# Kernel optimization log

Measured on AMD Instinct MI355X. Metric: run time of the kernel, lower is better.

## Reference

```python
import jax, jax.numpy as jnp
import numpy as np

DIM = 512
NUM_HEAD = 8
HEAD_DIM = DIM // NUM_HEAD
FFN = 4 * DIM


def setup_inputs() -> dict:
    key = jax.random.key(0)
    ks = jax.random.split(key, 16)
    s = DIM ** -0.5
    inp = {
        "x": jax.random.normal(ks[0], (4, 2048, DIM), jnp.float32),
        "wq": jax.random.normal(ks[1], (DIM, DIM), jnp.float32) * s,
        "bq": jnp.zeros((DIM,), jnp.float32),
        "wk": jax.random.normal(ks[2], (DIM, DIM), jnp.float32) * s,
        "bk": jnp.zeros((DIM,), jnp.float32),
        "wv": jax.random.normal(ks[3], (DIM, DIM), jnp.float32) * s,
        "bv": jnp.zeros((DIM,), jnp.float32),
        "wo": jax.random.normal(ks[4], (DIM, DIM), jnp.float32) * s,
        "bo": jnp.zeros((DIM,), jnp.float32),
        "w1": jax.random.normal(ks[5], (DIM, FFN), jnp.float32) * s,
        "b1": jnp.zeros((FFN,), jnp.float32),
        "w2": jax.random.normal(ks[6], (FFN, DIM), jnp.float32) * (FFN ** -0.5),
        "b2": jnp.zeros((DIM,), jnp.float32),
        "g1": jnp.ones((DIM,), jnp.float32),
        "be1": jnp.zeros((DIM,), jnp.float32),
        "g2": jnp.ones((DIM,), jnp.float32),
        "be2": jnp.zeros((DIM,), jnp.float32),
    }
    return inp


def layer_norm(x, g, b, eps=1e-5):
    mu = jnp.mean(x, axis=-1, keepdims=True)
    var = jnp.var(x, axis=-1, keepdims=True)
    return (x - mu) * jax.lax.rsqrt(var + eps) * g + b


def _forward(x, wq, bq, wk, bk, wv, bv, wo, bo, w1, b1, w2, b2, g1, be1, g2, be2):
    b, n, _ = x.shape
    scale = HEAD_DIM ** -0.5
    q = (x @ wq + bq).reshape(b, n, NUM_HEAD, HEAD_DIM).transpose(0, 2, 1, 3)
    k = (x @ wk + bk).reshape(b, n, NUM_HEAD, HEAD_DIM).transpose(0, 2, 1, 3)
    v = (x @ wv + bv).reshape(b, n, NUM_HEAD, HEAD_DIM).transpose(0, 2, 1, 3)
    scores = jnp.einsum('bhqd,bhkd->bhqk', q, k) * scale
    attn = jax.nn.softmax(scores, axis=-1)
    out = jnp.einsum('bhqk,bhkd->bhqd', attn, v)
    out = out.transpose(0, 2, 1, 3).reshape(b, n, DIM)
    out = out @ wo + bo
    x = layer_norm(out + x, g1, be1)
    h = jax.nn.gelu(x @ w1 + b1, approximate=False)
    ff = h @ w2 + b2
    x = layer_norm(ff + x, g2, be2)
    return x


def reference(x, wq, bq, wk, bk, wv, bv, wo, bo, w1, b1, w2, b2, g1, be1, g2, be2):
    return _forward(x, wq, bq, wk, bk, wv, bv, wo, bo, w1, b1, w2, b2, g1, be1, g2, be2)
```

## Files before the change

### kernel.cpp

```cpp
#include <hip/hip_runtime.h>
#include <math.h>

#define DIM 512
#define NHEAD 8
#define HD 64
#define FFN_DIM 2048
#define BATCH 4
#define SEQ 2048
#define MTOK (BATCH*SEQ)

typedef __attribute__((ext_vector_type(8))) short bf16x8;
typedef __attribute__((ext_vector_type(4))) float f32x4;

__device__ __forceinline__ unsigned short f2b(float f){
    unsigned int u = __float_as_uint(f);
    u += 0x7fffu + ((u >> 16) & 1u);
    return (unsigned short)(u >> 16);
}
__device__ __forceinline__ float b2f(unsigned short u){
    return __uint_as_float(((unsigned int)u) << 16);
}
__device__ __forceinline__ unsigned int pack_trunc(float f0, float f1){
    return __builtin_amdgcn_perm(__float_as_uint(f1), __float_as_uint(f0), 0x07060302u);
}
__device__ __forceinline__ void async_cp16(const unsigned short* g, unsigned short* l){
    __builtin_amdgcn_global_load_lds((const __attribute__((address_space(1))) unsigned int*)g,
                                     (__attribute__((address_space(3))) unsigned int*)l, 16, 0, 0);
}

__device__ __forceinline__ void transp32(const float* __restrict__ in, unsigned short* __restrict__ out,
                                         int N, int K, int n0_rd, int n0_wr, int k0,
                                         unsigned short (&t)[32][33], int tid){
    int tx = tid & 31, ty = tid >> 5;
    #pragma unroll
    for (int u = 0; u < 4; u++)
        t[tx][ty + 8*u] = f2b(in[(size_t)(k0 + ty + 8*u)*N + n0_rd + tx]);
    __syncthreads();
    #pragma unroll
    for (int u = 0; u < 4; u++)
        out[(size_t)(n0_wr + ty + 8*u)*K + k0 + tx] = t[ty + 8*u][tx];
}

__global__ void prep_kernel(const float* __restrict__ x,
                            const float* __restrict__ wq, const float* __restrict__ wk,
                            const float* __restrict__ wv, const float* __restrict__ wo,
                            const float* __restrict__ w1, const float* __restrict__ w2,
                            const float* __restrict__ bq, const float* __restrict__ bk,
                            const float* __restrict__ bv,
                            unsigned short* __restrict__ xb, unsigned short* __restrict__ wqkvT,
                            unsigned short* __restrict__ woT, unsigned short* __restrict__ w1T,
                            unsigned short* __restrict__ w2T, float* __restrict__ bqkv)
{
    __shared__ unsigned short t[32][33];
    int bid = blockIdx.x, tid = threadIdx.x;
    if (bid < 4096) {
        int i = (bid*256 + tid)*4;
        float4 v = *(const float4*)(x + i);
        ushort4 o; o.x=f2b(v.x); o.y=f2b(v.y); o.z=f2b(v.z); o.w=f2b(v.w);
        *(ushort4*)(xb + i) = o;
    } else if (bid < 4864) {
        int r = bid - 4096;
        int n0 = (r % 48)*32, k0 = (r / 48)*32;
        const float* w = (n0 < 512) ? wq : (n0 < 1024) ? wk : wv;
        transp32(w, wqkvT, 512, 512, n0 & 511, n0, k0, t, tid);
    } else if (bid < 5120) {
        int r = bid - 4864;
        int n0 = (r % 16)*32, k0 = (r / 16)*32;
        transp32(wo, woT, 512, 512, n0, n0, k0, t, tid);
    } else if (bid < 6144) {
        int r = bid - 5120;
        int n0 = (r % 64)*32, k0 = (r / 64)*32;
        transp32(w1, w1T, 2048, 512, n0, n0, k0, t, tid);
    } else if (bid < 7168) {
        int r = bid - 6144;
        int n0 = (r % 16)*32, k0 = (r / 16)*32;
        transp32(w2, w2T, 512, 2048, n0, n0, k0, t, tid);
    } else {
        int i = (bid - 7168)*256 + tid;
        if (i < 1536)
            bqkv[i] = (i < 512) ? bq[i] : (i < 1024) ? bk[i-512] : bv[i-1024];
    }
}

template<int MODE, int TN, int SK>
__global__ __launch_bounds__(256)
void gemm_bf16(const unsigned short* __restrict__ A, const unsigned short* __restrict__ Bt,
               const float* __restrict__ bias,
               float* __restrict__ Cf, unsigned short* __restrict__ Cb,
               unsigned short* __restrict__ qo, unsigned short* __restrict__ ko,
               unsigned short* __restrict__ vTo,
               int M, int N, int K)
{
    constexpr int JN = (TN == 128) ? 4 : 2;
    __shared__ unsigned short As[128*64];
    __shared__ unsigned short Bs[TN*64];
    int tid  = threadIdx.x;
    int lane = tid & 63;
    int ln = lane & 15, qd = lane >> 4;
    int m0 = blockIdx.x * 128, n0 = blockIdx.y * TN;
    int wid = tid >> 6;
    int wm = (wid >> 1) * 64;
    int wn = (wid & 1) * (16*JN);
    int kbeg = (SK > 1) ? (int)blockIdx.z * (K/SK) : 0;
    int kend = kbeg + K/SK;
    if (SK > 1) Cf += (size_t)blockIdx.z * M * N;

    f32x4 acc[4][JN];
    #pragma unroll
    for (int i = 0; i < 4; i++)
        #pragma unroll
        for (int j = 0; j < JN; j++) acc[i][j] = (f32x4){0.f,0.f,0.f,0.f};

    for (int k0 = kbeg; k0 < kend; k0 += 64) {
        #pragma unroll
        for (int i = 0; i < 4; i++) {
            int cid = i*256 + tid;
            int row = cid >> 3, cs = cid & 7;
            int cg = cs ^ (row & 7);
            async_cp16(&A[(size_t)(m0+row)*K + k0 + cg*8], &As[(cid & ~63) * 8]);
        }
        #pragma unroll
        for (int i = 0; i < TN/32; i++) {
            int cid = i*256 + tid;
            int row = cid >> 3, cs = cid & 7;
            int cg = cs ^ (row & 7);
            async_cp16(&Bt[(size_t)(n0+row)*K + k0 + cg*8], &Bs[(cid & ~63) * 8]);
        }
        __syncthreads();
        #pragma unroll
        for (int kk = 0; kk < 64; kk += 32) {
            int c0 = kk >> 3;
            bf16x8 af[4], bf[JN];
            #pragma unroll
            for (int t = 0; t < 4; t++)
                af[t] = *(bf16x8*)&As[(wm + t*16 + ln)*64 + ((c0 + qd) ^ (ln & 7))*8];
            #pragma unroll
            for (int t = 0; t < JN; t++)
                bf[t] = *(bf16x8*)&Bs[(wn + t*16 + ln)*64 + ((c0 + qd) ^ (ln & 7))*8];
            #pragma unroll
            for (int i = 0; i < 4; i++)
                #pragma unroll
                for (int j = 0; j < JN; j++)
                    acc[i][j] = __builtin_amdgcn_mfma_f32_16x16x32_bf16(af[i], bf[j], acc[i][j], 0,0,0);
        }
        __syncthreads();
    }

    const float QSCALE = 0.18033688011112042f;
    #pragma unroll
    for (int i = 0; i < 4; i++) {
        int mb = m0 + wm + i*16 + qd*4;
        #pragma unroll
        for (int j = 0; j < JN; j++) {
            int c = n0 + wn + j*16 + ln;
            float bv_ = (SK > 1 && blockIdx.z) ? 0.f : bias[c];
            float v[4];
            #pragma unroll
            for (int r = 0; r < 4; r++) v[r] = acc[i][j][r] + bv_;
            if (MODE == 0) {
                #pragma unroll
                for (int r = 0; r < 4; r++) Cf[(size_t)(mb+r)*N + c] = v[r];
            } else if (MODE == 2) {
                #pragma unroll
                for (int r = 0; r < 4; r++) {
                    float g = 0.5f * v[r] * (1.0f + erff(v[r] * 0.70710678118654752f));
                    Cb[(size_t)(mb+r)*N + c] = f2b(g);
                }
            } else {
                int b = mb >> 11, t0 = mb & 2047;
                if (c < 512) {
                    int h = c >> 6, hd = c & 63;
                    #pragma unroll
                    for (int r = 0; r < 4; r++)
                        qo[(((size_t)(b*8 + h))*SEQ + t0 + r)*64 + hd] = f2b(v[r] * QSCALE);
                } else if (c < 1024) {
                    int cc = c - 512, h = cc >> 6, hd = cc & 63;
                    #pragma unroll
                    for (int r = 0; r < 4; r++)
                        ko[(((size_t)(b*8 + h))*SEQ + t0 + r)*64 + hd] = f2b(v[r]);
                } else {
                    int cc = c - 1024, h = cc >> 6, hd = cc & 63;
                    ushort4 pk;
                    pk.x = f2b(v[0]); pk.y = f2b(v[1]); pk.z = f2b(v[2]); pk.w = f2b(v[3]);
                    *(ushort4*)&vTo[(((size_t)(b*8 + h))*64 + hd)*SEQ + t0] = pk;
                }
            }
        }
    }
}

__global__ __launch_bounds__(256)
void attn_mfma(const unsigned short* __restrict__ Q, const unsigned short* __restrict__ K,
               const unsigned short* __restrict__ VT, unsigned short* __restrict__ O)
{
    __shared__ unsigned short lds[20480];
    unsigned short* Qs = lds + 8192;
    unsigned short* Ps = lds + 16384;
    int tid  = threadIdx.x;
    int wid  = tid >> 6, lane = tid & 63;
    int ln = lane & 15, qd = lane >> 4;
    int qb = blockIdx.x, bh = blockIdx.y;

    #pragma unroll
    for (int i = 0; i < 2; i++) {
        int cid = i*256 + tid;
        int row = cid >> 3, cs = cid & 7;
        int cg = cs ^ (row & 7);
        async_cp16(&Q [((size_t)bh*SEQ + qb*64 + row)*64 + cg*8], &Qs[(cid & ~63)*8]);
        async_cp16(&K [((size_t)bh*SEQ + row)*64 + cg*8],         &lds[(cid & ~63)*8]);
        async_cp16(&VT[((size_t)bh*64 + row)*SEQ + cg*8],         &lds[4096 + (cid & ~63)*8]);
    }
    __syncthreads();

    bf16x8 qf[2];
    #pragma unroll
    for (int kk = 0; kk < 2; kk++)
        qf[kk] = *(bf16x8*)&Qs[(wid*16 + ln)*64 + (((kk*4) + qd) ^ (ln & 7))*8];
    __syncthreads();

    f32x4 o[4];
    #pragma unroll
    for (int dt = 0; dt < 4; dt++) o[dt] = (f32x4){0.f,0.f,0.f,0.f};
    float l_i = 0.f;

    for (int kt = 0; kt < 32; kt++) {
        int kof = (kt & 1) * 8192;
        int vof = 4096 + kof;
        if (kt < 31) {
            int nkof = 8192 - kof;
            #pragma unroll
            for (int i = 0; i < 2; i++) {
                int cid = i*256 + tid;
                int row = cid >> 3, cs = cid & 7;
                int cg = cs ^ (row & 7);
                async_cp16(&K [((size_t)bh*SEQ + (kt+1)*64 + row)*64 + cg*8], &lds[nkof + (cid & ~63)*8]);
                async_cp16(&VT[((size_t)bh*64 + row)*SEQ + (kt+1)*64 + cg*8], &lds[nkof + 4096 + (cid & ~63)*8]);
            }
        }

        f32x4 s[4];
        #pragma unroll
        for (int nt = 0; nt < 4; nt++) s[nt] = (f32x4){0.f,0.f,0.f,0.f};
        #pragma unroll
        for (int kk = 0; kk < 64; kk += 32) {
            int c0 = kk >> 3;
            #pragma unroll
            for (int nt = 0; nt < 4; nt++) {
                bf16x8 kf = *(bf16x8*)&lds[kof + (nt*16 + ln)*64 + ((c0 + qd) ^ (ln & 7))*8];
                s[nt] = __builtin_amdgcn_mfma_f32_16x16x32_bf16(kf, qf[kk>>5], s[nt], 0,0,0);
            }
        }

        #pragma unroll
        for (int nt = 0; nt < 4; nt++) {
            #pragma unroll
            for (int r = 0; r < 4; r++) {
                float p = __builtin_amdgcn_exp2f(s[nt][r]);
                s[nt][r] = p;
                l_i += p;
            }
        }

        #pragma unroll
        for (int nt = 0; nt < 4; nt++) {
            uint2 pk;
            pk.x = pack_trunc(s[nt][0], s[nt][1]);
            pk.y = pack_trunc(s[nt][2], s[nt][3]);
            *(uint2*)&Ps[(wid*16 + ln)*64 + ((nt*2 + (qd>>1)) ^ (ln & 7))*8 + (qd&1)*4] = pk;
        }

        #pragma unroll
        for (int kk = 0; kk < 64; kk += 32) {
            int c0 = kk >> 3;
            bf16x8 pf = *(bf16x8*)&Ps[(wid*16 + ln)*64 + ((c0 + qd) ^ (ln & 7))*8];
            #pragma unroll
            for (int dt = 0; dt < 4; dt++) {
                bf16x8 vf = *(bf16x8*)&lds[vof + (dt*16 + ln)*64 + ((c0 + qd) ^ (ln & 7))*8];
                o[dt] = __builtin_amdgcn_mfma_f32_16x16x32_bf16(vf, pf, o[dt], 0,0,0);
            }
        }
        __syncthreads();
    }

    l_i += __shfl_xor(l_i, 16);
    l_i += __shfl_xor(l_i, 32);
    float linv = 1.0f / l_i;

    int b = bh >> 3, h = bh & 7;
    int t = qb*64 + wid*16 + ln;
    #pragma unroll
    for (int dt = 0; dt < 4; dt++) {
        ushort4 pk;
        pk.x = f2b(o[dt][0]*linv); pk.y = f2b(o[dt][1]*linv);
        pk.z = f2b(o[dt][2]*linv); pk.w = f2b(o[dt][3]*linv);
        *(ushort4*)&O[((size_t)b*SEQ + t)*DIM + h*64 + dt*16 + qd*4] = pk;
    }
}

__global__ void ln1_kernel(const float* __restrict__ mainp, const float* __restrict__ resp,
                           const float* __restrict__ g, const float* __restrict__ be,
                           unsigned short* __restrict__ outb)
{
    int row  = blockIdx.x*4 + (threadIdx.x >> 6);
    int lane = threadIdx.x & 63;
    size_t base = (size_t)row * DIM + lane*8;

    float4 m0 = *(const float4*)(mainp + base);
    float4 m1 = *(const float4*)(mainp + base + 4);
    float4 r0 = *(const float4*)(resp + base);
    float4 r1 = *(const float4*)(resp + base + 4);
    float v[8] = { m0.x+r0.x, m0.y+r0.y, m0.z+r0.z, m0.w+r0.w,
                   m1.x+r1.x, m1.y+r1.y, m1.z+r1.z, m1.w+r1.w };
    float s = 0.f, s2 = 0.f;
    #pragma unroll
    for (int i = 0; i < 8; i++) { s += v[i]; s2 += v[i]*v[i]; }
    #pragma unroll
    for (int d = 32; d >= 1; d >>= 1) { s += __shfl_xor(s, d); s2 += __shfl_xor(s2, d); }
    float mean = s * (1.0f / DIM);
    float rstd = rsqrtf(s2 * (1.0f / DIM) - mean*mean + 1e-5f);

    float4 g0 = *(const float4*)(g + lane*8);
    float4 g1 = *(const float4*)(g + lane*8 + 4);
    float4 b0 = *(const float4*)(be + lane*8);
    float4 b1 = *(const float4*)(be + lane*8 + 4);
    float gg[8] = {g0.x,g0.y,g0.z,g0.w,g1.x,g1.y,g1.z,g1.w};
    float bb[8] = {b0.x,b0.y,b0.z,b0.w,b1.x,b1.y,b1.z,b1.w};
    ushort4 p0, p1;
    float o0 = (v[0]-mean)*rstd*gg[0]+bb[0], o1 = (v[1]-mean)*rstd*gg[1]+bb[1];
    float o2 = (v[2]-mean)*rstd*gg[2]+bb[2], o3 = (v[3]-mean)*rstd*gg[3]+bb[3];
    float o4 = (v[4]-mean)*rstd*gg[4]+bb[4], o5 = (v[5]-mean)*rstd*gg[5]+bb[5];
    float o6 = (v[6]-mean)*rstd*gg[6]+bb[6], o7 = (v[7]-mean)*rstd*gg[7]+bb[7];
    p0.x=f2b(o0); p0.y=f2b(o1); p0.z=f2b(o2); p0.w=f2b(o3);
    p1.x=f2b(o4); p1.y=f2b(o5); p1.z=f2b(o6); p1.w=f2b(o7);
    *(ushort4*)(outb + base)     = p0;
    *(ushort4*)(outb + base + 4) = p1;
}

__global__ void ln2_kernel(const float* __restrict__ m0p, const float* __restrict__ m1p,
                           const unsigned short* __restrict__ resb,
                           const float* __restrict__ g, const float* __restrict__ be,
                           float* __restrict__ outf)
{
    int row  = blockIdx.x*4 + (threadIdx.x >> 6);
    int lane = threadIdx.x & 63;
    size_t base = (size_t)row * DIM + lane*8;

    float4 a0 = *(const float4*)(m0p + base);
    float4 a1 = *(const float4*)(m0p + base + 4);
    float4 c0 = *(const float4*)(m1p + base);
    float4 c1 = *(const float4*)(m1p + base + 4);
    ushort4 rb0 = *(const ushort4*)(resb + base);
    ushort4 rb1 = *(const ushort4*)(resb + base + 4);
    float v[8] = { a0.x+c0.x+b2f(rb0.x), a0.y+c0.y+b2f(rb0.y),
                   a0.z+c0.z+b2f(rb0.z), a0.w+c0.w+b2f(rb0.w),
                   a1.x+c1.x+b2f(rb1.x), a1.y+c1.y+b2f(rb1.y),
                   a1.z+c1.z+b2f(rb1.z), a1.w+c1.w+b2f(rb1.w) };
    float s = 0.f, s2 = 0.f;
    #pragma unroll
    for (int i = 0; i < 8; i++) { s += v[i]; s2 += v[i]*v[i]; }
    #pragma unroll
    for (int d = 32; d >= 1; d >>= 1) { s += __shfl_xor(s, d); s2 += __shfl_xor(s2, d); }
    float mean = s * (1.0f / DIM);
    float rstd = rsqrtf(s2 * (1.0f / DIM) - mean*mean + 1e-5f);

    float4 g0 = *(const float4*)(g + lane*8);
    float4 g1 = *(const float4*)(g + lane*8 + 4);
    float4 b0 = *(const float4*)(be + lane*8);
    float4 b1 = *(const float4*)(be + lane*8 + 4);
    float gg[8] = {g0.x,g0.y,g0.z,g0.w,g1.x,g1.y,g1.z,g1.w};
    float bb[8] = {b0.x,b0.y,b0.z,b0.w,b1.x,b1.y,b1.z,b1.w};
    float o[8];
    #pragma unroll
    for (int i = 0; i < 8; i++) o[i] = (v[i] - mean)*rstd*gg[i] + bb[i];
    *(float4*)(outf + base)     = (float4){o[0],o[1],o[2],o[3]};
    *(float4*)(outf + base + 4) = (float4){o[4],o[5],o[6],o[7]};
}

extern "C" void kernel_launch(void* const* d_in, const int* in_sizes, int n_in,
                              void* d_out, int out_size, void* d_ws, size_t ws_size,
                              hipStream_t stream) {
    const float* x   = (const float*)d_in[0];
    const float* wq  = (const float*)d_in[1];
    const float* bq  = (const float*)d_in[2];
    const float* wk  = (const float*)d_in[3];
    const float* bk  = (const float*)d_in[4];
    const float* wv  = (const float*)d_in[5];
    const float* bv  = (const float*)d_in[6];
    const float* wo  = (const float*)d_in[7];
    const float* bo  = (const float*)d_in[8];
    const float* w1  = (const float*)d_in[9];
    const float* b1  = (const float*)d_in[10];
    const float* w2  = (const float*)d_in[11];
    const float* b2  = (const float*)d_in[12];
    const float* g1  = (const float*)d_in[13];
    const float* be1 = (const float*)d_in[14];
    const float* g2  = (const float*)d_in[15];
    const float* be2 = (const float*)d_in[16];
    float* out = (float*)d_out;

    char* w = (char*)d_ws;
    size_t off = 0;
    auto alloc = [&](size_t bytes){ void* p = w + off; off += (bytes + 255) & ~(size_t)255; return p; };
    unsigned short* xb     = (unsigned short*)alloc((size_t)MTOK*DIM*2);
    unsigned short* wqkvT  = (unsigned short*)alloc((size_t)1536*512*2);
    unsigned short* woT    = (unsigned short*)alloc((size_t)512*512*2);
    unsigned short* w1T    = (unsigned short*)alloc((size_t)2048*512*2);
    unsigned short* w2T    = (unsigned short*)alloc((size_t)512*2048*2);
    float*          bqkv   = (float*)alloc(1536*4);
    unsigned short* qb_    = (unsigned short*)alloc((size_t)32*SEQ*64*2);
    unsigned short* kb_    = (unsigned short*)alloc((size_t)32*SEQ*64*2);
    unsigned short* vT_    = (unsigned short*)alloc((size_t)32*64*SEQ*2);
    unsigned short* attno  = (unsigned short*)alloc((size_t)MTOK*DIM*2);
    float*          aproj  = (float*)alloc((size_t)MTOK*DIM*4);
    unsigned short* x1b    = (unsigned short*)alloc((size_t)MTOK*DIM*2);
    unsigned short* h_     = (unsigned short*)alloc((size_t)MTOK*FFN_DIM*2);
    float*          ff     = (float*)alloc((size_t)2*MTOK*DIM*4);

    prep_kernel<<<7174, 256, 0, stream>>>(x, wq, wk, wv, wo, w1, w2, bq, bk, bv,
                                          xb, wqkvT, woT, w1T, w2T, bqkv);

    gemm_bf16<1,128,1><<<dim3(64,12), 256, 0, stream>>>(xb, wqkvT, bqkv, nullptr, nullptr,
                                                        qb_, kb_, vT_, MTOK, 1536, DIM);
    attn_mfma<<<dim3(32,32), 256, 0, stream>>>(qb_, kb_, vT_, attno);
    gemm_bf16<0,64,1><<<dim3(64,8), 256, 0, stream>>>(attno, woT, bo, aproj, nullptr,
                                                      nullptr, nullptr, nullptr, MTOK, DIM, DIM);
    ln1_kernel<<<MTOK/4, 256, 0, stream>>>(aproj, x, g1, be1, x1b);
    gemm_bf16<2,128,1><<<dim3(64,16), 256, 0, stream>>>(x1b, w1T, b1, nullptr, h_,
                                                        nullptr, nullptr, nullptr, MTOK, FFN_DIM, DIM);
    gemm_bf16<0,128,2><<<dim3(64,4,2), 256, 0, stream>>>(h_, w2T, b2, ff, nullptr,
                                                         nullptr, nullptr, nullptr, MTOK, DIM, FFN_DIM);
    ln2_kernel<<<MTOK/4, 256, 0, stream>>>(ff, ff + (size_t)MTOK*DIM, x1b, g2, be2, out);
}
```

Baseline: 278.5 us.

## Process 128 queries per attention block and split-K the output projection

The attention kernel now gives each wave two 16-row query sub-tiles, so every K and V fragment loaded from LDS feeds two MFMAs. This halves the grid and the K/V traffic per query. The output projection GEMM switches to the 128-tile split-K-by-2 variant that writes two partial buffers, and LN1 now sums both partials plus the residual. The cost is more registers per wave and fewer blocks in flight for attention, plus an extra fp32 partial read in LN1.

```diff
diff --git a/kernel.cpp b/kernel.cpp
--- a/kernel.cpp
+++ b/kernel.cpp
@@ -193,7 +193,7 @@
 void attn_mfma(const unsigned short* __restrict__ Q, const unsigned short* __restrict__ K,
                const unsigned short* __restrict__ VT, unsigned short* __restrict__ O)
 {
-    __shared__ unsigned short lds[20480];
+    __shared__ unsigned short lds[24576];
     unsigned short* Qs = lds + 8192;
     unsigned short* Ps = lds + 16384;
     int tid  = threadIdx.x;
@@ -202,26 +202,36 @@
     int qb = blockIdx.x, bh = blockIdx.y;
 
     #pragma unroll
+    for (int i = 0; i < 4; i++) {
+        int cid = i*256 + tid;
+        int row = cid >> 3, cs = cid & 7;
+        int cg = cs ^ (row & 7);
+        async_cp16(&Q[((size_t)bh*SEQ + qb*128 + row)*64 + cg*8], &Qs[(cid & ~63)*8]);
+    }
+    #pragma unroll
     for (int i = 0; i < 2; i++) {
         int cid = i*256 + tid;
         int row = cid >> 3, cs = cid & 7;
         int cg = cs ^ (row & 7);
-        async_cp16(&Q [((size_t)bh*SEQ + qb*64 + row)*64 + cg*8], &Qs[(cid & ~63)*8]);
-        async_cp16(&K [((size_t)bh*SEQ + row)*64 + cg*8],         &lds[(cid & ~63)*8]);
-        async_cp16(&VT[((size_t)bh*64 + row)*SEQ + cg*8],         &lds[4096 + (cid & ~63)*8]);
+        async_cp16(&K [((size_t)bh*SEQ + row)*64 + cg*8], &lds[(cid & ~63)*8]);
+        async_cp16(&VT[((size_t)bh*64 + row)*SEQ + cg*8], &lds[4096 + (cid & ~63)*8]);
     }
     __syncthreads();
 
-    bf16x8 qf[2];
-    #pragma unroll
-    for (int kk = 0; kk < 2; kk++)
-        qf[kk] = *(bf16x8*)&Qs[(wid*16 + ln)*64 + (((kk*4) + qd) ^ (ln & 7))*8];
+    bf16x8 qf[2][2];
+    #pragma unroll
+    for (int qs = 0; qs < 2; qs++)
+        #pragma unroll
+        for (int kk = 0; kk < 2; kk++)
+            qf[qs][kk] = *(bf16x8*)&Qs[(wid*32 + qs*16 + ln)*64 + ((kk*4 + qd) ^ (ln & 7))*8];
     __syncthreads();
 
-    f32x4 o[4];
-    #pragma unroll
-    for (int dt = 0; dt < 4; dt++) o[dt] = (f32x4){0.f,0.f,0.f,0.f};
-    float l_i = 0.f;
+    f32x4 o[2][4];
+    #pragma unroll
+    for (int qs = 0; qs < 2; qs++)
+        #pragma unroll
+        for (int dt = 0; dt < 4; dt++) o[qs][dt] = (f32x4){0.f,0.f,0.f,0.f};
+    float l_i[2] = {0.f, 0.f};
 
     for (int kt = 0; kt < 32; kt++) {
         int kof = (kt & 1) * 8192;
@@ -238,66 +248,72 @@
             }
         }
 
-        f32x4 s[4];
-        #pragma unroll
-        for (int nt = 0; nt < 4; nt++) s[nt] = (f32x4){0.f,0.f,0.f,0.f};
-        #pragma unroll
-        for (int kk = 0; kk < 64; kk += 32) {
-            int c0 = kk >> 3;
+        f32x4 s[2][4];
+        #pragma unroll
+        for (int qs = 0; qs < 2; qs++)
+            #pragma unroll
+            for (int nt = 0; nt < 4; nt++) s[qs][nt] = (f32x4){0.f,0.f,0.f,0.f};
+        #pragma unroll
+        for (int kk = 0; kk < 2; kk++) {
             #pragma unroll
             for (int nt = 0; nt < 4; nt++) {
-                bf16x8 kf = *(bf16x8*)&lds[kof + (nt*16 + ln)*64 + ((c0 + qd) ^ (ln & 7))*8];
-                s[nt] = __builtin_amdgcn_mfma_f32_16x16x32_bf16(kf, qf[kk>>5], s[nt], 0,0,0);
+                bf16x8 kf = *(bf16x8*)&lds[kof + (nt*16 + ln)*64 + ((kk*4 + qd) ^ (ln & 7))*8];
+                s[0][nt] = __builtin_amdgcn_mfma_f32_16x16x32_bf16(kf, qf[0][kk], s[0][nt], 0,0,0);
+                s[1][nt] = __builtin_amdgcn_mfma_f32_16x16x32_bf16(kf, qf[1][kk], s[1][nt], 0,0,0);
             }
         }
 
         #pragma unroll
-        for (int nt = 0; nt < 4; nt++) {
-            #pragma unroll
-            for (int r = 0; r < 4; r++) {
-                float p = __builtin_amdgcn_exp2f(s[nt][r]);
-                s[nt][r] = p;
-                l_i += p;
+        for (int qs = 0; qs < 2; qs++) {
+            #pragma unroll
+            for (int nt = 0; nt < 4; nt++) {
+                #pragma unroll
+                for (int r = 0; r < 4; r++) {
+                    float p = __builtin_amdgcn_exp2f(s[qs][nt][r]);
+                    s[qs][nt][r] = p;
+                    l_i[qs] += p;
+                }
+                uint2 pk;
+                pk.x = pack_trunc(s[qs][nt][0], s[qs][nt][1]);
+                pk.y = pack_trunc(s[qs][nt][2], s[qs][nt][3]);
+                *(uint2*)&Ps[(wid*32 + qs*16 + ln)*64 + ((nt*2 + (qd>>1)) ^ (ln & 7))*8 + (qd&1)*4] = pk;
             }
         }
 
         #pragma unroll
-        for (int nt = 0; nt < 4; nt++) {
-            uint2 pk;
-            pk.x = pack_trunc(s[nt][0], s[nt][1]);
-            pk.y = pack_trunc(s[nt][2], s[nt][3]);
-            *(uint2*)&Ps[(wid*16 + ln)*64 + ((nt*2 + (qd>>1)) ^ (ln & 7))*8 + (qd&1)*4] = pk;
-        }
-
-        #pragma unroll
-        for (int kk = 0; kk < 64; kk += 32) {
-            int c0 = kk >> 3;
-            bf16x8 pf = *(bf16x8*)&Ps[(wid*16 + ln)*64 + ((c0 + qd) ^ (ln & 7))*8];
+        for (int kk = 0; kk < 2; kk++) {
+            bf16x8 pf0 = *(bf16x8*)&Ps[(wid*32 + ln)*64      + ((kk*4 + qd) ^ (ln & 7))*8];
+            bf16x8 pf1 = *(bf16x8*)&Ps[(wid*32 + 16 + ln)*64 + ((kk*4 + qd) ^ (ln & 7))*8];
             #pragma unroll
             for (int dt = 0; dt < 4; dt++) {
-                bf16x8 vf = *(bf16x8*)&lds[vof + (dt*16 + ln)*64 + ((c0 + qd) ^ (ln & 7))*8];
-                o[dt] = __builtin_amdgcn_mfma_f32_16x16x32_bf16(vf, pf, o[dt], 0,0,0);
+                bf16x8 vf = *(bf16x8*)&lds[vof + (dt*16 + ln)*64 + ((kk*4 + qd) ^ (ln & 7))*8];
+                o[0][dt] = __builtin_amdgcn_mfma_f32_16x16x32_bf16(vf, pf0, o[0][dt], 0,0,0);
+                o[1][dt] = __builtin_amdgcn_mfma_f32_16x16x32_bf16(vf, pf1, o[1][dt], 0,0,0);
             }
         }
         __syncthreads();
     }
 
-    l_i += __shfl_xor(l_i, 16);
-    l_i += __shfl_xor(l_i, 32);
-    float linv = 1.0f / l_i;
-
     int b = bh >> 3, h = bh & 7;
-    int t = qb*64 + wid*16 + ln;
-    #pragma unroll
-    for (int dt = 0; dt < 4; dt++) {
-        ushort4 pk;
-        pk.x = f2b(o[dt][0]*linv); pk.y = f2b(o[dt][1]*linv);
-        pk.z = f2b(o[dt][2]*linv); pk.w = f2b(o[dt][3]*linv);
-        *(ushort4*)&O[((size_t)b*SEQ + t)*DIM + h*64 + dt*16 + qd*4] = pk;
-    }
-}
-
-__global__ void ln1_kernel(const float* __restrict__ mainp, const float* __restrict__ resp,
+    #pragma unroll
+    for (int qs = 0; qs < 2; qs++) {
+        float l = l_i[qs];
+        l += __shfl_xor(l, 16);
+        l += __shfl_xor(l, 32);
+        float linv = 1.0f / l;
+        int t = qb*128 + wid*32 + qs*16 + ln;
+        #pragma unroll
+        for (int dt = 0; dt < 4; dt++) {
+            ushort4 pk;
+            pk.x = f2b(o[qs][dt][0]*linv); pk.y = f2b(o[qs][dt][1]*linv);
+            pk.z = f2b(o[qs][dt][2]*linv); pk.w = f2b(o[qs][dt][3]*linv);
+            *(ushort4*)&O[((size_t)b*SEQ + t)*DIM + h*64 + dt*16 + qd*4] = pk;
+        }
+    }
+}
+
+__global__ void ln1_kernel(const float* __restrict__ m0p, const float* __restrict__ m1p,
+                           const float* __restrict__ resp,
                            const float* __restrict__ g, const float* __restrict__ be,
                            unsigned short* __restrict__ outb)
 {
@@ -305,12 +321,14 @@
     int lane = threadIdx.x & 63;
     size_t base = (size_t)row * DIM + lane*8;
 
-    float4 m0 = *(const float4*)(mainp + base);
-    float4 m1 = *(const float4*)(mainp + base + 4);
+    float4 a0 = *(const float4*)(m0p + base);
+    float4 a1 = *(const float4*)(m0p + base + 4);
+    float4 c0 = *(const float4*)(m1p + base);
+    float4 c1 = *(const float4*)(m1p + base + 4);
     float4 r0 = *(const float4*)(resp + base);
     float4 r1 = *(const float4*)(resp + base + 4);
-    float v[8] = { m0.x+r0.x, m0.y+r0.y, m0.z+r0.z, m0.w+r0.w,
-                   m1.x+r1.x, m1.y+r1.y, m1.z+r1.z, m1.w+r1.w };
+    float v[8] = { a0.x+c0.x+r0.x, a0.y+c0.y+r0.y, a0.z+c0.z+r0.z, a0.w+c0.w+r0.w,
+                   a1.x+c1.x+r1.x, a1.y+c1.y+r1.y, a1.z+c1.z+r1.z, a1.w+c1.w+r1.w };
     float s = 0.f, s2 = 0.f;
     #pragma unroll
     for (int i = 0; i < 8; i++) { s += v[i]; s2 += v[i]*v[i]; }
@@ -326,12 +344,11 @@
     float gg[8] = {g0.x,g0.y,g0.z,g0.w,g1.x,g1.y,g1.z,g1.w};
     float bb[8] = {b0.x,b0.y,b0.z,b0.w,b1.x,b1.y,b1.z,b1.w};
     ushort4 p0, p1;
-    float o0 = (v[0]-mean)*rstd*gg[0]+bb[0], o1 = (v[1]-mean)*rstd*gg[1]+bb[1];
-    float o2 = (v[2]-mean)*rstd*gg[2]+bb[2], o3 = (v[3]-mean)*rstd*gg[3]+bb[3];
-    float o4 = (v[4]-mean)*rstd*gg[4]+bb[4], o5 = (v[5]-mean)*rstd*gg[5]+bb[5];
-    float o6 = (v[6]-mean)*rstd*gg[6]+bb[6], o7 = (v[7]-mean)*rstd*gg[7]+bb[7];
-    p0.x=f2b(o0); p0.y=f2b(o1); p0.z=f2b(o2); p0.w=f2b(o3);
-    p1.x=f2b(o4); p1.y=f2b(o5); p1.z=f2b(o6); p1.w=f2b(o7);
+    float o[8];
+    #pragma unroll
+    for (int i = 0; i < 8; i++) o[i] = (v[i]-mean)*rstd*gg[i] + bb[i];
+    p0.x=f2b(o[0]); p0.y=f2b(o[1]); p0.z=f2b(o[2]); p0.w=f2b(o[3]);
+    p1.x=f2b(o[4]); p1.y=f2b(o[5]); p1.z=f2b(o[6]); p1.w=f2b(o[7]);
     *(ushort4*)(outb + base)     = p0;
     *(ushort4*)(outb + base + 4) = p1;
 }
@@ -411,7 +428,6 @@
     unsigned short* kb_    = (unsigned short*)alloc((size_t)32*SEQ*64*2);
     unsigned short* vT_    = (unsigned short*)alloc((size_t)32*64*SEQ*2);
     unsigned short* attno  = (unsigned short*)alloc((size_t)MTOK*DIM*2);
-    float*          aproj  = (float*)alloc((size_t)MTOK*DIM*4);
     unsigned short* x1b    = (unsigned short*)alloc((size_t)MTOK*DIM*2);
     unsigned short* h_     = (unsigned short*)alloc((size_t)MTOK*FFN_DIM*2);
     float*          ff     = (float*)alloc((size_t)2*MTOK*DIM*4);
@@ -421,10 +437,10 @@
 
     gemm_bf16<1,128,1><<<dim3(64,12), 256, 0, stream>>>(xb, wqkvT, bqkv, nullptr, nullptr,
                                                         qb_, kb_, vT_, MTOK, 1536, DIM);
-    attn_mfma<<<dim3(32,32), 256, 0, stream>>>(qb_, kb_, vT_, attno);
-    gemm_bf16<0,64,1><<<dim3(64,8), 256, 0, stream>>>(attno, woT, bo, aproj, nullptr,
-                                                      nullptr, nullptr, nullptr, MTOK, DIM, DIM);
-    ln1_kernel<<<MTOK/4, 256, 0, stream>>>(aproj, x, g1, be1, x1b);
+    attn_mfma<<<dim3(16,32), 256, 0, stream>>>(qb_, kb_, vT_, attno);
+    gemm_bf16<0,128,2><<<dim3(64,4,2), 256, 0, stream>>>(attno, woT, bo, ff, nullptr,
+                                                         nullptr, nullptr, nullptr, MTOK, DIM, DIM);
+    ln1_kernel<<<MTOK/4, 256, 0, stream>>>(ff, ff + (size_t)MTOK*DIM, x, g1, be1, x1b);
     gemm_bf16<2,128,1><<<dim3(64,16), 256, 0, stream>>>(x1b, w1T, b1, nullptr, h_,
                                                         nullptr, nullptr, nullptr, MTOK, FFN_DIM, DIM);
     gemm_bf16<0,128,2><<<dim3(64,4,2), 256, 0, stream>>>(h_, w2T, b2, ff, nullptr,
```

New measurement: 272.4 us. 1.02x faster.
